# Performance work log

Measured on AMD Instinct MI355X. Metric: run time of the kernel, lower is better.

Reference implementation:

```python
import jax, jax.numpy as jnp
import numpy as np

ALPHA = 100.0  # self.softmax_alpha


def _interp_nearest(x, size):
    # torch F.interpolate mode='nearest': src_idx = floor(dst_idx * H_in / H_out)
    H, W = x.shape[-2], x.shape[-1]
    h, w = size
    ri = (jnp.arange(h) * H) // h
    ci = (jnp.arange(w) * W) // w
    return x[:, :, ri, :][:, :, :, ci]


def _interp_bilinear_ac(x, size):
    # torch F.interpolate mode='bilinear', align_corners=True
    H, W = x.shape[-2], x.shape[-1]
    h, w = size

    def coords(n_out, n_in):
        if n_out == 1:
            return jnp.zeros((1,), jnp.float32)
        return jnp.arange(n_out, dtype=jnp.float32) * ((n_in - 1) / (n_out - 1))

    ry, rx = coords(h, H), coords(w, W)
    y0 = jnp.floor(ry).astype(jnp.int32)
    x0 = jnp.floor(rx).astype(jnp.int32)
    y1 = jnp.clip(y0 + 1, 0, H - 1)
    x1 = jnp.clip(x0 + 1, 0, W - 1)
    wy = (ry - y0.astype(jnp.float32))[None, None, :, None]
    wx = (rx - x0.astype(jnp.float32))[None, None, None, :]
    rows = x[:, :, y0, :] * (1.0 - wy) + x[:, :, y1, :] * wy  # (n,c,h,W)
    return rows[:, :, :, x0] * (1.0 - wx) + rows[:, :, :, x1] * wx  # (n,c,h,w)


def _warp(unalign_fb, fa, fa_parse, fb, fb_parse, alpha):
    n, c, h, w = fa.shape
    c2 = unalign_fb.shape[1]
    hw = h * w
    # center and channel-normalize features per spatial location
    fa = fa - jnp.mean(fa, axis=(2, 3), keepdims=True)
    fb = fb - jnp.mean(fb, axis=(2, 3), keepdims=True)
    fa = fa.reshape(n, c, hw)
    fb = fb.reshape(n, c, hw)
    fa = fa / jnp.linalg.norm(fa, axis=1, keepdims=True)
    fb = fb / jnp.linalg.norm(fb, axis=1, keepdims=True)
    ufb = unalign_fb.reshape(n, c2, hw)
    mask_a = (fa_parse.reshape(n, -1, hw)[:, 1:, :] != 0).astype(fa.dtype)  # (n,K,hw)
    mask_b = (fb_parse.reshape(n, -1, hw)[:, 1:, :] != 0).astype(fb.dtype)
    local_fa = fa[:, None, :, :] * mask_a[:, :, None, :]  # (n,K,c,hw)
    local_fb = fb[:, None, :, :] * mask_b[:, :, None, :]  # (n,K,c,hw)
    # energy[n,k,q,p] = sum_c local_fb[n,k,c,q] * local_fa[n,k,c,p]
    energy = jnp.einsum('nkcq,nkcp->nkqp', local_fb, local_fa) * alpha
    corr = jax.nn.softmax(energy, axis=2)  # softmax over fb locations q
    warped = jnp.einsum('ncq,nkqp->nkcp', ufb, corr)  # (n,K,c2,hw)
    combined = (warped * mask_a[:, :, None, :]).sum(axis=1)  # (n,c2,hw)
    norm = jnp.maximum(mask_a.sum(axis=1, keepdims=True), 1.0)  # (n,1,hw)
    aligned = combined / norm
    return aligned.reshape(n, c2, h, w)


def setup_inputs() -> dict:
    key = jax.random.key(0)
    k1, k2, k3, k4, k5 = jax.random.split(key, 5)
    return {
        'unalign_fb': jax.random.normal(k1, (1, 64, 256, 256), jnp.float32),
        'fa': jax.random.normal(k2, (1, 256, 64, 64), jnp.float32),
        'fa_parse': jax.random.randint(k3, (1, 4, 256, 256), 0, 2).astype(jnp.int32),
        'fb': jax.random.normal(k4, (1, 256, 64, 64), jnp.float32),
        'fb_parse': jax.random.randint(k5, (1, 4, 256, 256), 0, 2).astype(jnp.int32),
    }


def reference(unalign_fb, fa, fa_parse, fb, fb_parse):
    raw_hw = unalign_fb.shape[-2:]
    feat_hw = fa.shape[-2:]
    fa_p = _interp_nearest(fa_parse, feat_hw)
    fb_p = _interp_nearest(fb_parse, feat_hw)
    ufb = _interp_bilinear_ac(unalign_fb, fb.shape[-2:])
    aligned = _warp(ufb, fa, fa_p, fb, fb_p, ALPHA)
    return _interp_bilinear_ac(aligned, raw_hw)
```

## Files before the change

### kernel.cpp

```cpp
#include <hip/hip_runtime.h>
#include <math.h>

#define HW 4096
#define CC 256
#define C2 64
#define E50f 1.928749848e-22f

typedef unsigned short USH;
typedef __attribute__((ext_vector_type(8))) _Float16 f16x8;
typedef __attribute__((ext_vector_type(8))) short bf8;
typedef __attribute__((ext_vector_type(4))) float f32x4;

__device__ __forceinline__ USH f2bf(float x) {
    unsigned u = __float_as_uint(x);
    u += 0x7fff + ((u >> 16) & 1);
    return (USH)(u >> 16);
}
__device__ __forceinline__ USH f2h(float x) {
    _Float16 h = (_Float16)x;
    return *(USH*)&h;
}
__device__ __forceinline__ float h2f(USH u) {
    _Float16 h = *(_Float16*)&u;
    return (float)h;
}

__device__ __forceinline__ void gl2lds16(const USH* g, USH* l) {
    __builtin_amdgcn_global_load_lds(
        (const __attribute__((address_space(1))) void*)g,
        (__attribute__((address_space(3))) void*)l, 16, 0, 0);
}

__global__ __launch_bounds__(256) void k_prep(
    const float* __restrict__ fa, const float* __restrict__ fb,
    USH* __restrict__ faT, USH* __restrict__ fbT,
    float* __restrict__ Sxx, float* __restrict__ colsum,
    const float* __restrict__ ufb_src, const int* __restrict__ fb_parse,
    USH* __restrict__ vtT, float* __restrict__ bgp) {
    __shared__ float tile[64][68];
    __shared__ float cs[64][4];
    __shared__ float sx[64][4];
    __shared__ float4 sred[256];
    int t = threadIdx.x;
    if (blockIdx.x < 128) {
        int which = blockIdx.x & 1;
        int pblk = blockIdx.x >> 1;
        int p0 = pblk * 64;
        const float* src = which ? fb : fa;
        USH* dst = which ? fbT : faT;
        int c_r = t >> 2, seg = t & 3;
        float sxx_acc = 0.f;
        for (int ci = 0; ci < 4; ++ci) {
            int c0 = ci * 64;
            float lsum = 0.f;
            {
                const float* s = &src[(size_t)(c0 + c_r) * HW + p0 + seg * 16];
#pragma unroll
                for (int k = 0; k < 4; ++k) {
                    float4 v = *(const float4*)&s[k * 4];
                    *(float4*)&tile[c_r][seg * 16 + k * 4] = v;
                    lsum += v.x + v.y + v.z + v.w;
                }
            }
            cs[c_r][seg] = lsum;
            __syncthreads();
            if (t < 64)
                colsum[(which * 64 + pblk) * 256 + c0 + t] =
                    cs[t][0] + cs[t][1] + cs[t][2] + cs[t][3];
            {
                int p_r = c_r;
                int cl = seg * 16;
                union { USH us[8]; uint4 v; } h0, h1;
#pragma unroll
                for (int j = 0; j < 8; ++j) {
                    USH h = f2h(tile[cl + j][p_r]);
                    float xv = h2f(h);
                    sxx_acc += xv * xv;
                    h0.us[j] = h;
                }
#pragma unroll
                for (int j = 0; j < 8; ++j) {
                    USH h = f2h(tile[cl + 8 + j][p_r]);
                    float xv = h2f(h);
                    sxx_acc += xv * xv;
                    h1.us[j] = h;
                }
                int kc = ci * 2 + (seg >> 1);
                size_t base = (size_t)kc * 131072 + (size_t)(p0 + p_r) * 32 + (seg & 1) * 16;
                *(uint4*)&dst[base] = h0.v;
                *(uint4*)&dst[base + 8] = h1.v;
            }
            __syncthreads();
        }
        sx[c_r][seg] = sxx_acc;
        __syncthreads();
        if (t < 64)
            Sxx[which * HW + p0 + t] = sx[t][0] + sx[t][1] + sx[t][2] + sx[t][3];
        return;
    }
    int bid = blockIdx.x - 128;
    int pblk = bid & 15, c = bid >> 4;
    int p = pblk * 256 + t;
    int j = p >> 6, i = p & 63;
    int off = (4 * j) * 256 + 4 * i;
    float m0 = (fb_parse[1 * 65536 + off] != 0) ? 1.f : 0.f;
    float m1 = (fb_parse[2 * 65536 + off] != 0) ? 1.f : 0.f;
    float m2 = (fb_parse[3 * 65536 + off] != 0) ? 1.f : 0.f;
    float ry = j * (255.0f / 63.0f);
    int y0 = (int)ry; y0 = min(y0, 255); int y1 = min(y0 + 1, 255);
    float wy = ry - (float)y0;
    float rx = i * (255.0f / 63.0f);
    int x0 = (int)rx; x0 = min(x0, 255); int x1 = min(x0 + 1, 255);
    float wx = rx - (float)x0;
    const float* sc = ufb_src + c * 65536;
    float r0 = sc[y0 * 256 + x0] * (1.f - wx) + sc[y0 * 256 + x1] * wx;
    float r1 = sc[y1 * 256 + x0] * (1.f - wx) + sc[y1 * 256 + x1] * wx;
    float v = r0 * (1.f - wy) + r1 * wy;
    size_t cbase = (size_t)(p >> 5) * 8192 + (p & 31);
    vtT[cbase + (0 * 65 + c) * 32] = f2bf(v * m0);
    vtT[cbase + (1 * 65 + c) * 32] = f2bf(v * m1);
    vtT[cbase + (2 * 65 + c) * 32] = f2bf(v * m2);
    if (c == 0) {
        vtT[cbase + 64 * 32]  = f2bf(m0);
        vtT[cbase + 129 * 32] = f2bf(m1);
        vtT[cbase + 194 * 32] = f2bf(m2);
        for (int m = 195; m < 256; ++m) vtT[cbase + m * 32] = 0;
    }
    sred[t] = make_float4(v, v * m0, v * m1, v * m2);
    __syncthreads();
    for (int st = 128; st > 0; st >>= 1) {
        if (t < st) {
            float4 o = sred[t + st];
            sred[t].x += o.x; sred[t].y += o.y; sred[t].z += o.z; sred[t].w += o.w;
        }
        __syncthreads();
    }
    if (t == 0) {
        float4 r = sred[0];
        bgp[pblk * 320 + 256 + c]     = r.x;
        bgp[pblk * 320 + 0 * 65 + c]  = r.y;
        bgp[pblk * 320 + 1 * 65 + c]  = r.z;
        bgp[pblk * 320 + 2 * 65 + c]  = r.w;
    }
    __syncthreads();
    if (c == 0) {
        sred[t] = make_float4(m0, m1, m2, 0.f);
        __syncthreads();
        for (int st = 128; st > 0; st >>= 1) {
            if (t < st) {
                float4 o = sred[t + st];
                sred[t].x += o.x; sred[t].y += o.y; sred[t].z += o.z;
            }
            __syncthreads();
        }
        if (t == 0) {
            float4 r = sred[0];
            bgp[pblk * 320 + 64]  = r.x;
            bgp[pblk * 320 + 129] = r.y;
            bgp[pblk * 320 + 194] = r.z;
        }
    }
}

__global__ void k_stats(const float* __restrict__ colsum, float* __restrict__ stats) {
    __shared__ float4 sred[256];
    int t = threadIdx.x;
    float s0 = 0.f, s1 = 0.f;
    for (int pb = 0; pb < 64; ++pb) {
        s0 += colsum[(0 * 64 + pb) * 256 + t];
        s1 += colsum[(1 * 64 + pb) * 256 + t];
    }
    float mu0 = s0 * (1.0f / HW), mu1 = s1 * (1.0f / HW);
    stats[t] = mu0;
    stats[256 + t] = mu1;
    sred[t] = make_float4(mu0 * mu1, mu0 * mu0, mu1 * mu1, 0.f);
    __syncthreads();
    for (int st = 128; st > 0; st >>= 1) {
        if (t < st) {
            float4 o = sred[t + st];
            sred[t].x += o.x; sred[t].y += o.y; sred[t].z += o.z;
        }
        __syncthreads();
    }
    if (t == 0) {
        stats[512] = sred[0].x;
        stats[513] = sred[0].y;
        stats[514] = sred[0].z;
    }
}

__global__ void k_corr(const USH* __restrict__ faT, const USH* __restrict__ fbT,
                       const float* __restrict__ Sxx, const float* __restrict__ stats,
                       float* __restrict__ dra) {
    __shared__ float smu[512];
    __shared__ float scc[4];
    int t = threadIdx.x;
    int which = blockIdx.y;
    smu[t] = stats[t];
    smu[256 + t] = stats[256 + t];
    if (t < 3) scc[t] = stats[512 + t];
    __syncthreads();
    int p = blockIdx.x * 256 + t;
    const USH* xT = which ? fbT : faT;
    const float* mu_self = &smu[which * 256];
    const float* mu_oth  = &smu[(1 - which) * 256];
    float ca = 0.f, da = 0.f;
    for (int kc = 0; kc < 8; ++kc) {
        union { uint4 v; USH us[8]; } u[4];
        size_t base = (size_t)kc * 131072 + (size_t)p * 32;
#pragma unroll
        for (int g = 0; g < 4; ++g) u[g].v = *(const uint4*)&xT[base + g * 8];
#pragma unroll
        for (int g = 0; g < 4; ++g)
#pragma unroll
            for (int jj = 0; jj < 8; ++jj) {
                float xv = h2f(u[g].us[jj]);
                int c = kc * 32 + g * 8 + jj;
                ca += xv * mu_self[c];
                da += xv * mu_oth[c];
            }
    }
    float Sself = scc[1 + which];
    float ra = rsqrtf(Sxx[which * HW + p] - 2.f * ca + Sself);
    dra[which * HW + p] = da;
    dra[2 * HW + which * HW + p] = ra;
}

__global__ __launch_bounds__(256, 3) void k_attn(
    const USH* __restrict__ faT, const USH* __restrict__ fbT,
    const USH* __restrict__ vtT, const float* __restrict__ dra,
    const float* __restrict__ stats, float* __restrict__ part) {
    __shared__ USH sA[2][2048];
    __shared__ USH sB[2][4096];
    __shared__ USH sE[64 * 136];
    int t = threadIdx.x;
    int p0 = blockIdx.x * 64;
    int z = blockIdx.y;
    int w = t >> 6, lane = t & 63, lr = lane & 15, quad = lane >> 4;
    f32x4 accp[4][4] = {};

    const USH* gA = faT + (size_t)p0 * 32;
    float Kc = stats[512];
    float da4[4], ra4[4];
#pragma unroll
    for (int jj = 0; jj < 4; ++jj) {
        da4[jj] = dra[p0 + 16 * jj + lr];
        ra4[jj] = dra[2 * HW + p0 + 16 * jj + lr];
    }

#define DMA_AB(buf, kc, q0)                                                          \
    do {                                                                             \
        gl2lds16(gA + (size_t)(kc) * 131072 + w * 512 + lane * 8, &sA[buf][w * 512]);\
        _Pragma("unroll")                                                            \
        for (int cc = 0; cc < 2; ++cc)                                               \
            gl2lds16(fbT + (size_t)(kc) * 131072 + (size_t)(q0) * 32 +               \
                         (2 * w + cc) * 512 + lane * 8,                              \
                     &sB[buf][(2 * w + cc) * 512]);                                  \
    } while (0)

    DMA_AB(0, 0, z * 512);
    __syncthreads();
    for (int qt = 0; qt < 4; ++qt) {
        int q0 = z * 512 + qt * 128;
        f32x4 accs[2][4] = {};
        for (int kc = 0; kc < 8; ++kc) {
            int cur = kc & 1;
            if (kc < 7)      DMA_AB(cur ^ 1, kc + 1, q0);
            else if (qt < 3) DMA_AB(0, 0, q0 + 128);
            f16x8 a[2], b[4];
#pragma unroll
            for (int i = 0; i < 2; ++i)
                a[i] = *(const f16x8*)&sB[cur][(32 * w + 16 * i + lr) * 32 + quad * 8];
#pragma unroll
            for (int jj = 0; jj < 4; ++jj)
                b[jj] = *(const f16x8*)&sA[cur][(16 * jj + lr) * 32 + quad * 8];
#pragma unroll
            for (int i = 0; i < 2; ++i)
#pragma unroll
                for (int jj = 0; jj < 4; ++jj)
                    accs[i][jj] = __builtin_amdgcn_mfma_f32_16x16x32_f16(a[i], b[jj], accs[i][jj], 0, 0, 0);
            __syncthreads();
        }
#pragma unroll
        for (int i = 0; i < 2; ++i) {
            int qb = q0 + 32 * w + 16 * i + 4 * quad;
            float4 db4 = *(const float4*)&dra[HW + qb];
            float4 rb4 = *(const float4*)&dra[3 * HW + qb];
#pragma unroll
            for (int jj = 0; jj < 4; ++jj) {
                float rr = ra4[jj];
                float dd = da4[jj] - Kc;
                float s0 = (accs[i][jj][0] - dd - db4.x) * (rr * rb4.x);
                float s1 = (accs[i][jj][1] - dd - db4.y) * (rr * rb4.y);
                float s2 = (accs[i][jj][2] - dd - db4.z) * (rr * rb4.z);
                float s3 = (accs[i][jj][3] - dd - db4.w) * (rr * rb4.w);
                unsigned u0 = ((unsigned)f2bf(__expf(fmaf(100.f, s1, -50.f))) << 16)
                            | (unsigned)f2bf(__expf(fmaf(100.f, s0, -50.f)));
                unsigned u1 = ((unsigned)f2bf(__expf(fmaf(100.f, s3, -50.f))) << 16)
                            | (unsigned)f2bf(__expf(fmaf(100.f, s2, -50.f)));
                int addr = (16 * jj + lr) * 136 + 32 * w + 16 * i + 4 * quad;
                uint2 u; u.x = u0; u.y = u1;
                *(uint2*)&sE[addr] = u;
            }
        }
        __syncthreads();
#pragma unroll
        for (int kc = 0; kc < 4; ++kc) {
            size_t vbase = (size_t)(z * 16 + qt * 4 + kc) * 8192 + (size_t)quad * 8;
            bf8 av[4], be[4];
#pragma unroll
            for (int i = 0; i < 4; ++i)
                av[i] = *(const bf8*)&vtT[vbase + (64 * w + 16 * i + lr) * 32];
#pragma unroll
            for (int jj = 0; jj < 4; ++jj)
                be[jj] = *(const bf8*)&sE[(16 * jj + lr) * 136 + kc * 32 + quad * 8];
#pragma unroll
            for (int i = 0; i < 4; ++i)
#pragma unroll
                for (int jj = 0; jj < 4; ++jj)
                    accp[i][jj] = __builtin_amdgcn_mfma_f32_16x16x32_bf16(av[i], be[jj], accp[i][jj], 0, 0, 0);
        }
        __syncthreads();
    }
#undef DMA_AB
    float* op = part + (size_t)z * 1048576;
#pragma unroll
    for (int i = 0; i < 4; ++i) {
        int m = 64 * w + 16 * i + quad * 4;
#pragma unroll
        for (int jj = 0; jj < 4; ++jj) {
            int pc = p0 + 16 * jj + lr;
#pragma unroll
            for (int r = 0; r < 4; ++r)
                op[(size_t)(m + r) * HW + pc] = accp[i][jj][r];
        }
    }
}

__global__ void k_combine8(const float* __restrict__ part, const float* __restrict__ bgp,
                           const int* __restrict__ fa_parse, float* __restrict__ aligned) {
    __shared__ float sums[8];
    int t = threadIdx.x;
    int c2 = blockIdx.y;
    if (t < 7) {
        int idx = (t < 3) ? (t * 65 + 64) : ((t < 6) ? (t - 3) * 65 + c2 : 256 + c2);
        float s = 0.f;
#pragma unroll
        for (int pb = 0; pb < 16; ++pb) s += bgp[pb * 320 + idx];
        sums[t] = s;
    }
    __syncthreads();
    int p = blockIdx.x * 256 + t;
    int jj = p >> 6, ii = p & 63;
    int off = (4 * jj) * 256 + 4 * ii;
    float num = 0.f, s = 0.f;
    for (int k = 0; k < 3; ++k) {
        float ma = (fa_parse[(k + 1) * 65536 + off] != 0) ? 1.f : 0.f;
        s += ma;
        float den = E50f * (4096.0f - sums[k]);
        float nu  = E50f * (sums[6] - sums[3 + k]);
        size_t rd = (size_t)(k * 65 + 64) * HW + p;
        size_t rn = (size_t)(k * 65 + c2) * HW + p;
#pragma unroll
        for (int z = 0; z < 8; ++z) {
            den += part[(size_t)z * 1048576 + rd];
            nu  += part[(size_t)z * 1048576 + rn];
        }
        num += ma * (nu / den);
    }
    aligned[c2 * HW + p] = num / fmaxf(s, 1.f);
}

__global__ void k_bilin_up(const float* __restrict__ aligned, float* __restrict__ out) {
    int idx = (blockIdx.x * 256 + threadIdx.x) * 4;
    int c2 = blockIdx.y;
    int y = idx >> 8;
    float ry = y * (63.0f / 255.0f);
    int y0 = (int)ry; y0 = min(y0, 63); int y1 = min(y0 + 1, 63);
    float wy = ry - (float)y0;
    const float* a = aligned + c2 * HW;
    float4 o;
    float* op = &o.x;
#pragma unroll
    for (int u = 0; u < 4; ++u) {
        int x = (idx & 255) + u;
        float rx = x * (63.0f / 255.0f);
        int x0 = (int)rx; x0 = min(x0, 63); int x1 = min(x0 + 1, 63);
        float wx = rx - (float)x0;
        float r0 = a[y0 * 64 + x0] * (1.f - wx) + a[y0 * 64 + x1] * wx;
        float r1 = a[y1 * 64 + x0] * (1.f - wx) + a[y1 * 64 + x1] * wx;
        op[u] = r0 * (1.f - wy) + r1 * wy;
    }
    *(float4*)&out[c2 * 65536 + idx] = o;
}

extern "C" void kernel_launch(void* const* d_in, const int* in_sizes, int n_in,
                              void* d_out, int out_size, void* d_ws, size_t ws_size,
                              hipStream_t stream) {
    const float* unalign_fb = (const float*)d_in[0];
    const float* fa         = (const float*)d_in[1];
    const int*   fa_parse   = (const int*)d_in[2];
    const float* fb         = (const float*)d_in[3];
    const int*   fb_parse   = (const int*)d_in[4];
    float* out = (float*)d_out;

    float* w = (float*)d_ws;
    float* stats   = w;
    float* colsum  = w + 1024;
    float* Sxx     = w + 33792;
    float* dra     = w + 41984;
    float* bgp     = w + 58368;
    float* part    = w + 63488;
    float* aligned = w + 8452096;
    USH* faT = (USH*)(w + 8714240);
    USH* fbT = (USH*)(w + 9238528);
    USH* vtT = (USH*)(w + 9762816);

    k_prep<<<dim3(1152), dim3(256), 0, stream>>>(fa, fb, faT, fbT, Sxx, colsum,
                                                 unalign_fb, fb_parse, vtT, bgp);
    k_stats<<<dim3(1), dim3(256), 0, stream>>>(colsum, stats);
    k_corr<<<dim3(16, 2), dim3(256), 0, stream>>>(faT, fbT, Sxx, stats, dra);
    k_attn<<<dim3(64, 8), dim3(256), 0, stream>>>(faT, fbT, vtT, dra, stats, part);
    k_combine8<<<dim3(16, 64), dim3(256), 0, stream>>>(part, bgp, fa_parse, aligned);
    k_bilin_up<<<dim3(64, 64), dim3(256), 0, stream>>>(aligned, out);
}
```

Before: 146.7 us.

## Load attention operands directly from global and fuse combine with bilinear upsample

```diff
diff --git a/kernel.cpp b/kernel.cpp
--- a/kernel.cpp
+++ b/kernel.cpp
@@ -23,12 +23,6 @@
 __device__ __forceinline__ float h2f(USH u) {
     _Float16 h = *(_Float16*)&u;
     return (float)h;
-}
-
-__device__ __forceinline__ void gl2lds16(const USH* g, USH* l) {
-    __builtin_amdgcn_global_load_lds(
-        (const __attribute__((address_space(1))) void*)g,
-        (__attribute__((address_space(3))) void*)l, 16, 0, 0);
 }
 
 __global__ __launch_bounds__(256) void k_prep(
@@ -230,8 +224,6 @@
     const USH* __restrict__ faT, const USH* __restrict__ fbT,
     const USH* __restrict__ vtT, const float* __restrict__ dra,
     const float* __restrict__ stats, float* __restrict__ part) {
-    __shared__ USH sA[2][2048];
-    __shared__ USH sB[2][4096];
     __shared__ USH sE[64 * 136];
     int t = threadIdx.x;
     int p0 = blockIdx.x * 64;
@@ -239,7 +231,6 @@
     int w = t >> 6, lane = t & 63, lr = lane & 15, quad = lane >> 4;
     f32x4 accp[4][4] = {};
 
-    const USH* gA = faT + (size_t)p0 * 32;
     float Kc = stats[512];
     float da4[4], ra4[4];
 #pragma unroll
@@ -248,39 +239,27 @@
         ra4[jj] = dra[2 * HW + p0 + 16 * jj + lr];
     }
 
-#define DMA_AB(buf, kc, q0)                                                          \
-    do {                                                                             \
-        gl2lds16(gA + (size_t)(kc) * 131072 + w * 512 + lane * 8, &sA[buf][w * 512]);\
-        _Pragma("unroll")                                                            \
-        for (int cc = 0; cc < 2; ++cc)                                               \
-            gl2lds16(fbT + (size_t)(kc) * 131072 + (size_t)(q0) * 32 +               \
-                         (2 * w + cc) * 512 + lane * 8,                              \
-                     &sB[buf][(2 * w + cc) * 512]);                                  \
-    } while (0)
-
-    DMA_AB(0, 0, z * 512);
-    __syncthreads();
     for (int qt = 0; qt < 4; ++qt) {
         int q0 = z * 512 + qt * 128;
         f32x4 accs[2][4] = {};
+#pragma unroll 2
         for (int kc = 0; kc < 8; ++kc) {
-            int cur = kc & 1;
-            if (kc < 7)      DMA_AB(cur ^ 1, kc + 1, q0);
-            else if (qt < 3) DMA_AB(0, 0, q0 + 128);
+            const USH* fbb = fbT + (size_t)kc * 131072 + (size_t)quad * 8;
+            const USH* fab = faT + (size_t)kc * 131072 + (size_t)quad * 8;
             f16x8 a[2], b[4];
 #pragma unroll
             for (int i = 0; i < 2; ++i)
-                a[i] = *(const f16x8*)&sB[cur][(32 * w + 16 * i + lr) * 32 + quad * 8];
+                a[i] = *(const f16x8*)&fbb[(size_t)(q0 + 32 * w + 16 * i + lr) * 32];
 #pragma unroll
             for (int jj = 0; jj < 4; ++jj)
-                b[jj] = *(const f16x8*)&sA[cur][(16 * jj + lr) * 32 + quad * 8];
+                b[jj] = *(const f16x8*)&fab[(size_t)(p0 + 16 * jj + lr) * 32];
 #pragma unroll
             for (int i = 0; i < 2; ++i)
 #pragma unroll
                 for (int jj = 0; jj < 4; ++jj)
                     accs[i][jj] = __builtin_amdgcn_mfma_f32_16x16x32_f16(a[i], b[jj], accs[i][jj], 0, 0, 0);
-            __syncthreads();
-        }
+        }
+        __syncthreads();
 #pragma unroll
         for (int i = 0; i < 2; ++i) {
             int qb = q0 + 32 * w + 16 * i + 4 * quad;
@@ -304,7 +283,7 @@
             }
         }
         __syncthreads();
-#pragma unroll
+#pragma unroll 2
         for (int kc = 0; kc < 4; ++kc) {
             size_t vbase = (size_t)(z * 16 + qt * 4 + kc) * 8192 + (size_t)quad * 8;
             bf8 av[4], be[4];
@@ -320,9 +299,7 @@
                 for (int jj = 0; jj < 4; ++jj)
                     accp[i][jj] = __builtin_amdgcn_mfma_f32_16x16x32_bf16(av[i], be[jj], accp[i][jj], 0, 0, 0);
         }
-        __syncthreads();
-    }
-#undef DMA_AB
+    }
     float* op = part + (size_t)z * 1048576;
 #pragma unroll
     for (int i = 0; i < 4; ++i) {
@@ -337,11 +314,14 @@
     }
 }
 
-__global__ void k_combine8(const float* __restrict__ part, const float* __restrict__ bgp,
-                           const int* __restrict__ fa_parse, float* __restrict__ aligned) {
+__global__ void k_combine_up(const float* __restrict__ part, const float* __restrict__ bgp,
+                             const int* __restrict__ fa_parse, float* __restrict__ out) {
+    __shared__ float sAl[10][64];
     __shared__ float sums[8];
     int t = threadIdx.x;
     int c2 = blockIdx.y;
+    int bx = blockIdx.x;
+    int ylo = (bx * 32 * 63) / 255;
     if (t < 7) {
         int idx = (t < 3) ? (t * 65 + 64) : ((t < 6) ? (t - 3) * 65 + c2 : 256 + c2);
         float s = 0.f;
@@ -350,48 +330,59 @@
         sums[t] = s;
     }
     __syncthreads();
-    int p = blockIdx.x * 256 + t;
-    int jj = p >> 6, ii = p & 63;
-    int off = (4 * jj) * 256 + 4 * ii;
-    float num = 0.f, s = 0.f;
-    for (int k = 0; k < 3; ++k) {
-        float ma = (fa_parse[(k + 1) * 65536 + off] != 0) ? 1.f : 0.f;
-        s += ma;
-        float den = E50f * (4096.0f - sums[k]);
-        float nu  = E50f * (sums[6] - sums[3 + k]);
-        size_t rd = (size_t)(k * 65 + 64) * HW + p;
-        size_t rn = (size_t)(k * 65 + c2) * HW + p;
-#pragma unroll
-        for (int z = 0; z < 8; ++z) {
-            den += part[(size_t)z * 1048576 + rd];
-            nu  += part[(size_t)z * 1048576 + rn];
-        }
-        num += ma * (nu / den);
-    }
-    aligned[c2 * HW + p] = num / fmaxf(s, 1.f);
-}
-
-__global__ void k_bilin_up(const float* __restrict__ aligned, float* __restrict__ out) {
-    int idx = (blockIdx.x * 256 + threadIdx.x) * 4;
-    int c2 = blockIdx.y;
-    int y = idx >> 8;
-    float ry = y * (63.0f / 255.0f);
-    int y0 = (int)ry; y0 = min(y0, 63); int y1 = min(y0 + 1, 63);
-    float wy = ry - (float)y0;
-    const float* a = aligned + c2 * HW;
-    float4 o;
-    float* op = &o.x;
-#pragma unroll
-    for (int u = 0; u < 4; ++u) {
-        int x = (idx & 255) + u;
-        float rx = x * (63.0f / 255.0f);
-        int x0 = (int)rx; x0 = min(x0, 63); int x1 = min(x0 + 1, 63);
-        float wx = rx - (float)x0;
-        float r0 = a[y0 * 64 + x0] * (1.f - wx) + a[y0 * 64 + x1] * wx;
-        float r1 = a[y1 * 64 + x0] * (1.f - wx) + a[y1 * 64 + x1] * wx;
-        op[u] = r0 * (1.f - wy) + r1 * wy;
-    }
-    *(float4*)&out[c2 * 65536 + idx] = o;
+#pragma unroll
+    for (int it = 0; it < 3; ++it) {
+        int v = it * 256 + t;
+        if (v < 640) {
+            int r = v >> 6, col = v & 63;
+            int row = ylo + r;
+            if (row < 64) {
+                int p = row * 64 + col;
+                int off = (4 * row) * 256 + 4 * col;
+                float num = 0.f, s = 0.f;
+                for (int k = 0; k < 3; ++k) {
+                    float ma = (fa_parse[(k + 1) * 65536 + off] != 0) ? 1.f : 0.f;
+                    s += ma;
+                    float den = E50f * (4096.0f - sums[k]);
+                    float nu  = E50f * (sums[6] - sums[3 + k]);
+                    size_t rd = (size_t)(k * 65 + 64) * HW + p;
+                    size_t rn = (size_t)(k * 65 + c2) * HW + p;
+#pragma unroll
+                    for (int zz = 0; zz < 8; ++zz) {
+                        den += part[(size_t)zz * 1048576 + rd];
+                        nu  += part[(size_t)zz * 1048576 + rn];
+                    }
+                    num += ma * (nu / den);
+                }
+                sAl[r][col] = num / fmaxf(s, 1.f);
+            }
+        }
+    }
+    __syncthreads();
+    int xg = (t & 63) * 4;
+    int yb = t >> 6;
+#pragma unroll
+    for (int it = 0; it < 8; ++it) {
+        int y = bx * 32 + yb + it * 4;
+        float ry = y * (63.0f / 255.0f);
+        int y0 = (int)ry; y0 = min(y0, 63); int y1 = min(y0 + 1, 63);
+        float wy = ry - (float)y0;
+        const float* a0 = sAl[y0 - ylo];
+        const float* a1 = sAl[y1 - ylo];
+        float4 o;
+        float* op = &o.x;
+#pragma unroll
+        for (int u = 0; u < 4; ++u) {
+            int x = xg + u;
+            float rx = x * (63.0f / 255.0f);
+            int x0 = (int)rx; x0 = min(x0, 63); int x1 = min(x0 + 1, 63);
+            float wx = rx - (float)x0;
+            float r0 = a0[x0] * (1.f - wx) + a0[x1] * wx;
+            float r1 = a1[x0] * (1.f - wx) + a1[x1] * wx;
+            op[u] = r0 * (1.f - wy) + r1 * wy;
+        }
+        *(float4*)&out[c2 * 65536 + y * 256 + xg] = o;
+    }
 }
 
 extern "C" void kernel_launch(void* const* d_in, const int* in_sizes, int n_in,
@@ -411,16 +402,14 @@
     float* dra     = w + 41984;
     float* bgp     = w + 58368;
     float* part    = w + 63488;
-    float* aligned = w + 8452096;
-    USH* faT = (USH*)(w + 8714240);
-    USH* fbT = (USH*)(w + 9238528);
-    USH* vtT = (USH*)(w + 9762816);
+    USH* faT = (USH*)(w + 8452096);
+    USH* fbT = (USH*)(w + 8976384);
+    USH* vtT = (USH*)(w + 9500672);
 
     k_prep<<<dim3(1152), dim3(256), 0, stream>>>(fa, fb, faT, fbT, Sxx, colsum,
                                                  unalign_fb, fb_parse, vtT, bgp);
     k_stats<<<dim3(1), dim3(256), 0, stream>>>(colsum, stats);
     k_corr<<<dim3(16, 2), dim3(256), 0, stream>>>(faT, fbT, Sxx, stats, dra);
     k_attn<<<dim3(64, 8), dim3(256), 0, stream>>>(faT, fbT, vtT, dra, stats, part);
-    k_combine8<<<dim3(16, 64), dim3(256), 0, stream>>>(part, bgp, fa_parse, aligned);
-    k_bilin_up<<<dim3(64, 64), dim3(256), 0, stream>>>(aligned, out);
-}
+    k_combine_up<<<dim3(8, 64), dim3(256), 0, stream>>>(part, bgp, fa_parse, out);
+}
```

Result: no change. 149.0 us (+1.6%).
